# Optimization experiments

Measured on AMD Instinct MI355X. Metric: run time of the kernel, lower is better.

Reference implementation:

```python
import jax, jax.numpy as jnp
import numpy as np

H = 8  # number_heads

def setup_inputs() -> dict:
    key = jax.random.key(0)
    ks = jax.random.split(key, 10)
    B, Nx, Ny, Qd, Kd, Vd = 4, 2048, 2048, 512, 512, 512
    s = 0.02
    return {
        "X": jax.random.normal(ks[0], (B, Nx, Qd), jnp.float32),
        "Y": jax.random.normal(ks[1], (B, Ny, Kd), jnp.float32),
        "Wq": jax.random.normal(ks[2], (Vd, Qd), jnp.float32) * s,
        "bq": jax.random.normal(ks[3], (Vd,), jnp.float32) * s,
        "Wk": jax.random.normal(ks[4], (Vd, Kd), jnp.float32) * s,
        "bk": jax.random.normal(ks[5], (Vd,), jnp.float32) * s,
        "Wv": jax.random.normal(ks[6], (Vd, Kd), jnp.float32) * s,
        "bv": jax.random.normal(ks[7], (Vd,), jnp.float32) * s,
        "Wo": jax.random.normal(ks[8], (Vd, Vd), jnp.float32) * s,
        "bo": jax.random.normal(ks[9], (Vd,), jnp.float32) * s,
    }

def reference(X, Y, Wq, bq, Wk, bk, Wv, bv, Wo, bo):
    B, Nq, _ = X.shape
    Nk = Y.shape[1]
    Vd = Wq.shape[0]
    d = Vd // H  # head dim (dim_split)
    # QKV projections (torch Linear: x @ W^T + b)
    Q = (X @ Wq.T + bq).reshape(B, Nq, H, d)
    K = (Y @ Wk.T + bk).reshape(B, Nk, H, d)
    V = (Y @ Wv.T + bv).reshape(B, Nk, H, d)
    # attention: softmax(Q K^T / sqrt(d)) per head
    scores = jnp.einsum("bqhd,bkhd->bhqk", Q, K) / jnp.sqrt(jnp.float32(d))
    attn = jax.nn.softmax(scores, axis=-1)
    # residual on Q (pre-output-proj), per the original: O = Q_split + Attn @ V_split
    O = Q + jnp.einsum("bhqk,bkhd->bqhd", attn, V)
    O = O.reshape(B, Nq, Vd)  # concat heads back
    return O @ Wo.T + bo
```

## Files before the change

kernel.cpp:

```cpp
#include <hip/hip_runtime.h>
#include <hip/hip_bf16.h>

typedef unsigned short u16;
typedef __attribute__((ext_vector_type(4))) float f32x4;
typedef __attribute__((ext_vector_type(16))) float f32x16;
typedef __attribute__((ext_vector_type(8))) short bf16x8;
typedef __attribute__((ext_vector_type(4))) int i32x4;
typedef __attribute__((ext_vector_type(4))) unsigned short u16x4;

#define DEVI static __device__ __forceinline__

DEVI u16 f2bf(float f) {
  __hip_bfloat16 h = __float2bfloat16(f);
  return *reinterpret_cast<u16*>(&h);
}
DEVI float bf2f(u16 u) {
  unsigned int x = ((unsigned int)u) << 16;
  return __uint_as_float(x);
}
DEVI float exp2a(float x) {
  float r;
  asm("v_exp_f32 %0, %1" : "=v"(r) : "v"(x));
  return r;
}
DEVI int cvtpk(float lo, float hi) {
  int r;
  asm("v_cvt_pk_bf16_f32 %0, %1, %2" : "=v"(r) : "v"(lo), "v"(hi));
  return r;
}
DEVI f32x16 mfma32(bf16x8 a, bf16x8 b, f32x16 c) {
  return __builtin_amdgcn_mfma_f32_32x32x16_bf16(a, b, c, 0, 0, 0);
}
DEVI float xhalf_sum(float x) {
  float a = x, b;
  asm volatile("v_mov_b32 %0, %1" : "=v"(b) : "v"(x));
  asm volatile("v_permlane32_swap_b32 %0, %1" : "+v"(a), "+v"(b));
  return a + b;
}

DEVI void gload_lds16(const void* g, void* l) {
  __builtin_amdgcn_global_load_lds(
      (const __attribute__((address_space(1))) unsigned int*)g,
      (__attribute__((address_space(3))) unsigned int*)l, 16, 0, 0);
}

#define BAR() __builtin_amdgcn_s_barrier()
#define WAITV0() asm volatile("s_waitcnt vmcnt(0)" ::: "memory")
#define WAITV4() asm volatile("s_waitcnt vmcnt(4)" ::: "memory")
#define WAITV8() asm volatile("s_waitcnt vmcnt(8)" ::: "memory")

__global__ __launch_bounds__(256) void k_convall(
    const float* __restrict__ X, const float* __restrict__ Y,
    const float* __restrict__ Wq, const float* __restrict__ Wk,
    const float* __restrict__ Wv, const float* __restrict__ Wo,
    u16* __restrict__ Xb, u16* __restrict__ Yb, u16* __restrict__ Wb) {
  long i = ((long)blockIdx.x * 256 + threadIdx.x) * 8;
  const float* s;
  u16* d;
  long off;
  if (i < 4194304) {
    s = X; d = Xb; off = i;
  } else if (i < 8388608) {
    s = Y; d = Yb; off = i - 4194304;
  } else {
    long w = (i - 8388608) >> 18;
    off = (i - 8388608) & 262143;
    s = w == 0 ? Wq : w == 1 ? Wk : w == 2 ? Wv : Wo;
    d = Wb + w * 262144;
  }
  f32x4 a = *(const f32x4*)(s + off);
  f32x4 b = *(const f32x4*)(s + off + 4);
  bf16x8 v;
#pragma unroll
  for (int j = 0; j < 4; ++j) {
    v[j]     = (short)f2bf(a[j]);
    v[4 + j] = (short)f2bf(b[j]);
  }
  *(bf16x8*)(d + off) = v;
}

struct GemmAcc { f32x4 acc[4][4]; };

DEVI void gemm_body(const u16* __restrict__ A, const u16* __restrict__ Bw,
                    int m0, int n0, char* sm, GemmAcc& G) {
  const int tid = threadIdx.x;
  const int wid = tid >> 6, lane = tid & 63;
  const int g = lane >> 4, li = lane & 15;
  const int wr = wid >> 1, wc = wid & 1;

  int arow[4], acol[4];
#pragma unroll
  for (int i = 0; i < 4; ++i) {
    int P0 = ((i * 4 + wid) << 10) + lane * 16;
    int L0 = P0 ^ (((P0 >> 7) & 7) << 4);
    arow[i] = L0 >> 7;
    acol[i] = L0 & 127;
  }

#pragma unroll
  for (int mr = 0; mr < 4; ++mr)
#pragma unroll
    for (int nr = 0; nr < 4; ++nr) G.acc[mr][nr] = (f32x4){0.f, 0.f, 0.f, 0.f};

  auto stage = [&](int kt, int half) {
    char* As = sm + half * 32768;
    char* Bs = As + 16384;
    const int k0b = kt * 128;
#pragma unroll
    for (int i = 0; i < 4; ++i)
      gload_lds16((const char*)A + (size_t)(m0 + arow[i]) * 1024 + k0b + acol[i],
                  As + ((i * 4 + wid) << 10));
#pragma unroll
    for (int i = 0; i < 4; ++i)
      gload_lds16((const char*)Bw + (size_t)(n0 + arow[i]) * 1024 + k0b + acol[i],
                  Bs + ((i * 4 + wid) << 10));
  };

  stage(0, 0);
#pragma unroll 1
  for (int kt = 0; kt < 8; ++kt) {
    const int half = kt & 1;
    if (kt < 7) {
      stage(kt + 1, half ^ 1);
      WAITV8();
    } else {
      WAITV0();
    }
    BAR();
    const char* As = sm + half * 32768;
    const char* Bs = As + 16384;
#pragma unroll
    for (int ks = 0; ks < 2; ++ks) {
      bf16x8 af[4], bfr[4];
#pragma unroll
      for (int mr = 0; mr < 4; ++mr) {
        int row = wr * 64 + mr * 16 + li;
        int L = row * 128 + ks * 64 + g * 16;
        int P = L ^ ((row & 7) << 4);
        af[mr] = *(const bf16x8*)(As + P);
      }
#pragma unroll
      for (int nr = 0; nr < 4; ++nr) {
        int row = wc * 64 + nr * 16 + li;
        int L = row * 128 + ks * 64 + g * 16;
        int P = L ^ ((row & 7) << 4);
        bfr[nr] = *(const bf16x8*)(Bs + P);
      }
#pragma unroll
      for (int mr = 0; mr < 4; ++mr)
#pragma unroll
        for (int nr = 0; nr < 4; ++nr)
          G.acc[mr][nr] = __builtin_amdgcn_mfma_f32_16x16x32_bf16(
              af[mr], bfr[nr], G.acc[mr][nr], 0, 0, 0);
    }
    BAR();
  }
}

__global__ __launch_bounds__(256) void k_gemm_qkv(
    const u16* __restrict__ Xb, const u16* __restrict__ Yb,
    const u16* __restrict__ Wall, const float* __restrict__ bq,
    const float* __restrict__ bk, const float* __restrict__ bv,
    u16* __restrict__ Qb, u16* __restrict__ Kb, u16* __restrict__ Vtb) {
  __shared__ __align__(16) char sm[65536];
  const int z = blockIdx.z;
  int lin = blockIdx.x + 4 * blockIdx.y;
  int xcd = lin & 7, slot = lin >> 3;

  const u16 *Ag, *Bg;
  int m0, n0;
  if (z == 2) {
    Ag = Wall + 2 * 262144;
    Bg = Yb;
    m0 = (slot & 3) * 128;
    n0 = (xcd * 8 + (slot >> 2)) * 128;
  } else {
    Ag = z ? Yb : Xb;
    Bg = Wall + (size_t)z * 262144;
    m0 = (xcd * 8 + (slot >> 2)) * 128;
    n0 = (slot & 3) * 128;
  }

  GemmAcc G;
  gemm_body(Ag, Bg, m0, n0, sm, G);

  const int tid = threadIdx.x;
  const int wid = tid >> 6, lane = tid & 63;
  const int g = lane >> 4, li = lane & 15;
  const int wr = wid >> 1, wc = wid & 1;

  if (z <= 1) {
    u16* Cout = z ? Kb : Qb;
    const float* bias = z ? bk : bq;
#pragma unroll
    for (int nr = 0; nr < 4; ++nr) {
      int col = n0 + wc * 64 + nr * 16 + li;
      float bvv = bias[col];
#pragma unroll
      for (int mr = 0; mr < 4; ++mr) {
#pragma unroll
        for (int j = 0; j < 4; ++j) {
          int row = m0 + wr * 64 + mr * 16 + g * 4 + j;
          float v = G.acc[mr][nr][j] + bvv;
          int b = row >> 11, nn = row & 2047, h = col >> 6, dd = col & 63;
          Cout[(((size_t)(b * 8 + h) << 11) + nn) * 64 + dd] = f2bf(v);
        }
      }
    }
  } else {
#pragma unroll
    for (int mr = 0; mr < 4; ++mr) {
#pragma unroll
      for (int j = 0; j < 4; ++j) {
        int row = m0 + wr * 64 + mr * 16 + g * 4 + j;
        float bvv = bv[row];
        int hh = row >> 6, dd = row & 63;
#pragma unroll
        for (int nr = 0; nr < 4; ++nr) {
          int col = n0 + wc * 64 + nr * 16 + li;
          int b = col >> 11, nn = col & 2047;
          Vtb[(((size_t)(b * 8 + hh) * 64) + dd) * 2048 + nn] =
              f2bf(G.acc[mr][nr][j] + bvv);
        }
      }
    }
  }
}

__global__ __launch_bounds__(256) void k_gemm_out(const u16* __restrict__ A,
                                                  const u16* __restrict__ Bw,
                                                  const float* __restrict__ bias,
                                                  float* __restrict__ Cout) {
  __shared__ __align__(16) char sm[65536];
  int lin = blockIdx.x + 4 * blockIdx.y;
  int xcd = lin & 7, slot = lin >> 3;
  int by = xcd * 8 + (slot >> 2), bx = slot & 3;
  const int m0 = by * 128, n0 = bx * 128;

  GemmAcc G;
  gemm_body(A, Bw, m0, n0, sm, G);

  const int tid = threadIdx.x;
  const int wid = tid >> 6, lane = tid & 63;
  const int g = lane >> 4, li = lane & 15;
  const int wr = wid >> 1, wc = wid & 1;
#pragma unroll
  for (int nr = 0; nr < 4; ++nr) {
    int col = n0 + wc * 64 + nr * 16 + li;
    float bvv = bias[col];
#pragma unroll
    for (int mr = 0; mr < 4; ++mr) {
#pragma unroll
      for (int j = 0; j < 4; ++j) {
        int row = m0 + wr * 64 + mr * 16 + g * 4 + j;
        Cout[(size_t)row * 512 + col] = G.acc[mr][nr][j] + bvv;
      }
    }
  }
}

DEVI void attn_phase(const char* L, int kb, int vb, const int* v4, int sv0, int sv1,
                     const bf16x8* qfA, const bf16x8* qfB,
                     f32x16& oA0, f32x16& oA1, f32x16& oB0, f32x16& oB1,
                     float& lsumA, float& lsumB) {
  const f32x16 Z = {};
  f32x16 sA, sB;
  bf16x8 kf;
  kf = *(const bf16x8*)(L + kb + v4[0]);
  sA = mfma32(kf, qfA[0], Z);  sB = mfma32(kf, qfB[0], Z);
  kf = *(const bf16x8*)(L + kb + v4[1]);
  sA = mfma32(kf, qfA[1], sA); sB = mfma32(kf, qfB[1], sB);
  kf = *(const bf16x8*)(L + kb + v4[2]);
  sA = mfma32(kf, qfA[2], sA); sB = mfma32(kf, qfB[2], sB);
  kf = *(const bf16x8*)(L + kb + v4[3]);
  sA = mfma32(kf, qfA[3], sA); sB = mfma32(kf, qfB[3], sB);

  bf16x8 va0l = *(const bf16x8*)(L + vb + v4[sv0]);
  bf16x8 va0h = *(const bf16x8*)(L + vb + 4096 + v4[sv0]);
  bf16x8 va1l = *(const bf16x8*)(L + vb + v4[sv1]);
  bf16x8 va1h = *(const bf16x8*)(L + vb + 4096 + v4[sv1]);

#pragma unroll
  for (int i = 0; i < 16; ++i) sA[i] = exp2a(sA[i]);
#pragma unroll
  for (int i = 0; i < 16; ++i) sB[i] = exp2a(sB[i]);
  float tA[4], tB[4];
#pragma unroll
  for (int i = 0; i < 4; ++i) {
    tA[i] = (sA[4 * i] + sA[4 * i + 1]) + (sA[4 * i + 2] + sA[4 * i + 3]);
    tB[i] = (sB[4 * i] + sB[4 * i + 1]) + (sB[4 * i + 2] + sB[4 * i + 3]);
  }
  lsumA += (tA[0] + tA[1]) + (tA[2] + tA[3]);
  lsumB += (tB[0] + tB[1]) + (tB[2] + tB[3]);

  bf16x8 pbA[2], pbB[2];
#pragma unroll
  for (int kt = 0; kt < 2; ++kt) {
    const int base = kt * 8;
    int a0 = cvtpk(sA[base + 0], sA[base + 1]);
    int a1 = cvtpk(sA[base + 2], sA[base + 3]);
    int b0 = cvtpk(sA[base + 4], sA[base + 5]);
    int b1 = cvtpk(sA[base + 6], sA[base + 7]);
    asm volatile("v_permlane32_swap_b32 %0, %1" : "+v"(a0), "+v"(b0));
    asm volatile("v_permlane32_swap_b32 %0, %1" : "+v"(a1), "+v"(b1));
    i32x4 pi = {a0, a1, b0, b1};
    pbA[kt] = __builtin_bit_cast(bf16x8, pi);
    int c0 = cvtpk(sB[base + 0], sB[base + 1]);
    int c1 = cvtpk(sB[base + 2], sB[base + 3]);
    int d0 = cvtpk(sB[base + 4], sB[base + 5]);
    int d1 = cvtpk(sB[base + 6], sB[base + 7]);
    asm volatile("v_permlane32_swap_b32 %0, %1" : "+v"(c0), "+v"(d0));
    asm volatile("v_permlane32_swap_b32 %0, %1" : "+v"(c1), "+v"(d1));
    i32x4 qi = {c0, c1, d0, d1};
    pbB[kt] = __builtin_bit_cast(bf16x8, qi);
  }

  oA0 = mfma32(va0l, pbA[0], oA0);
  oB0 = mfma32(va0l, pbB[0], oB0);
  oA1 = mfma32(va0h, pbA[0], oA1);
  oB1 = mfma32(va0h, pbB[0], oB1);
  oA0 = mfma32(va1l, pbA[1], oA0);
  oB0 = mfma32(va1l, pbB[1], oB0);
  oA1 = mfma32(va1h, pbA[1], oA1);
  oB1 = mfma32(va1h, pbB[1], oB1);
}

__global__ __launch_bounds__(512, 2) void k_attn(const u16* __restrict__ Qb,
                                                 const u16* __restrict__ Kb,
                                                 const u16* __restrict__ Vt,
                                                 u16* __restrict__ Ob) {
  __shared__ __align__(16) char lds[67584];
  const int tid = threadIdx.x, wid = tid >> 6, lane = tid & 63;
  const int li = lane & 31, h = lane >> 5;
  const int grp = wid >> 2, w4 = wid & 3;

  const int lin = blockIdx.x;
  const int xcd = lin & 7, slot = lin >> 3;
  const int bh = xcd * 4 + (slot >> 3);
  const int qt = slot & 7;
  const int start = (slot * 3) & 15;

  const u16* Qh = Qb + ((size_t)bh << 11) * 64;
  const u16* Kh = Kb + ((size_t)bh << 11) * 64;
  const u16* Vh = Vt + (size_t)bh * 64 * 2048;

  int v4[4];
  {
    const int swz = (li & 7) << 4;
#pragma unroll
    for (int s = 0; s < 4; ++s) v4[s] = li * 128 + ((s * 32 + h * 16) ^ swz);
  }

  const int qA = qt * 256 + w4 * 64 + li;
  const int qB = qA + 32;
  const float C2 = 0.18033688f;
  bf16x8 qfA[4], qfB[4];
#pragma unroll
  for (int k4 = 0; k4 < 4; ++k4) {
    bf16x8 fA = *(const bf16x8*)(Qh + (size_t)qA * 64 + k4 * 16 + h * 8);
    bf16x8 fB = *(const bf16x8*)(Qh + (size_t)qB * 64 + k4 * 16 + h * 8);
    bf16x8 rA, rB;
#pragma unroll
    for (int e = 0; e < 4; ++e) {
      int pA = cvtpk(bf2f((u16)fA[2 * e]) * C2, bf2f((u16)fA[2 * e + 1]) * C2);
      rA[2 * e]     = (short)(pA & 0xffff);
      rA[2 * e + 1] = (short)((unsigned)pA >> 16);
      int pB = cvtpk(bf2f((u16)fB[2 * e]) * C2, bf2f((u16)fB[2 * e + 1]) * C2);
      rB[2 * e]     = (short)(pB & 0xffff);
      rB[2 * e + 1] = (short)((unsigned)pB >> 16);
    }
    qfA[k4] = rA;
    qfB[k4] = rB;
  }

  char* gb = lds + grp * 32768;
  const char* Lg = gb;
  int ksrc[2], vsrc[2];
#pragma unroll
  for (int j = 0; j < 2; ++j) {
    int P0 = w4 * 2048 + j * 1024 + lane * 16;
    int L0 = P0 ^ (((P0 >> 7) & 7) << 4);
    ksrc[j] = L0;
    vsrc[j] = (L0 >> 7) * 4096 + (L0 & 127);
  }

  auto T = [&](int n) { return grp * 16 + ((start + n) & 15); };
  auto stage = [&](int tt, int bb) {
#pragma unroll
    for (int j = 0; j < 2; ++j)
      gload_lds16((const char*)Kh + (size_t)tt * 8192 + ksrc[j],
                  gb + bb + w4 * 2048 + j * 1024);
#pragma unroll
    for (int j = 0; j < 2; ++j)
      gload_lds16((const char*)Vh + (size_t)tt * 128 + vsrc[j],
                  gb + bb + 8192 + w4 * 2048 + j * 1024);
  };

  f32x16 oA0 = {}, oA1 = {}, oB0 = {}, oB1 = {};
  float lsumA = 0.f, lsumB = 0.f;

  stage(T(0), 0);
  stage(T(1), 16384);
  WAITV4();
  BAR();

#pragma unroll 1
  for (int it = 0; it < 14; ++it) {
    const int cur = (it & 1) * 16384;
    attn_phase(Lg, cur, cur + 8192, v4, 0, 1, qfA, qfB, oA0, oA1, oB0, oB1,
               lsumA, lsumB);
    attn_phase(Lg, cur + 4096, cur + 8192, v4, 2, 3, qfA, qfB, oA0, oA1, oB0, oB1,
               lsumA, lsumB);
    BAR();
    stage(T(it + 2), cur);
    WAITV4();
    BAR();
  }
  attn_phase(Lg, 0, 8192, v4, 0, 1, qfA, qfB, oA0, oA1, oB0, oB1, lsumA, lsumB);
  attn_phase(Lg, 4096, 8192, v4, 2, 3, qfA, qfB, oA0, oA1, oB0, oB1, lsumA, lsumB);
  WAITV0();
  BAR();
  attn_phase(Lg, 16384, 24576, v4, 0, 1, qfA, qfB, oA0, oA1, oB0, oB1, lsumA, lsumB);
  attn_phase(Lg, 20480, 24576, v4, 2, 3, qfA, qfB, oA0, oA1, oB0, oB1, lsumA, lsumB);

  __syncthreads();
  if (grp == 1) {
#pragma unroll
    for (int j = 0; j < 16; ++j) {
      const f32x16& o = (j < 4) ? oA0 : (j < 8) ? oA1 : (j < 12) ? oB0 : oB1;
      const int s2 = (j & 3) * 4;
      f32x4 c = {o[s2 + 0], o[s2 + 1], o[s2 + 2], o[s2 + 3]};
      *(f32x4*)(lds + w4 * 16384 + j * 1024 + lane * 16) = c;
    }
    ((float*)(lds + 65536))[w4 * 128 + lane] = lsumA;
    ((float*)(lds + 65536))[w4 * 128 + 64 + lane] = lsumB;
  }
  __syncthreads();
  if (grp == 0) {
#pragma unroll
    for (int j = 0; j < 16; ++j) {
      f32x4 c = *(const f32x4*)(lds + w4 * 16384 + j * 1024 + lane * 16);
      f32x16& o = (j < 4) ? oA0 : (j < 8) ? oA1 : (j < 12) ? oB0 : oB1;
      const int s2 = (j & 3) * 4;
      o[s2 + 0] += c[0]; o[s2 + 1] += c[1]; o[s2 + 2] += c[2]; o[s2 + 3] += c[3];
    }
    lsumA += ((const float*)(lds + 65536))[w4 * 128 + lane];
    lsumB += ((const float*)(lds + 65536))[w4 * 128 + 64 + lane];
    const float invA = 1.0f / xhalf_sum(lsumA);
    const float invB = 1.0f / xhalf_sum(lsumB);

    const int b = bh >> 3, head = bh & 7;
#pragma unroll
    for (int half = 0; half < 2; ++half) {
      const int q = half ? qB : qA;
      const float inv = half ? invB : invA;
      u16* orow = Ob + ((size_t)(b * 2048 + q)) * 512 + head * 64;
      const u16* qrow = Qh + (size_t)q * 64;
#pragma unroll
      for (int dt = 0; dt < 2; ++dt) {
        const f32x16& o = half ? (dt ? oB1 : oB0) : (dt ? oA1 : oA0);
#pragma unroll
        for (int s2 = 0; s2 < 4; ++s2) {
          int d0 = dt * 32 + s2 * 8 + h * 4;
          u16x4 qv = *(const u16x4*)(qrow + d0);
          u16x4 w;
#pragma unroll
          for (int j = 0; j < 4; ++j)
            w[j] = f2bf(fmaf(o[s2 * 4 + j], inv, bf2f(qv[j])));
          *(u16x4*)(orow + d0) = w;
        }
      }
    }
  }
}

extern "C" void kernel_launch(void* const* d_in, const int* in_sizes, int n_in,
                              void* d_out, int out_size, void* d_ws, size_t ws_size,
                              hipStream_t stream) {
  const float* X  = (const float*)d_in[0];
  const float* Y  = (const float*)d_in[1];
  const float* Wq = (const float*)d_in[2];
  const float* bq = (const float*)d_in[3];
  const float* Wk = (const float*)d_in[4];
  const float* bk = (const float*)d_in[5];
  const float* Wv = (const float*)d_in[6];
  const float* bv = (const float*)d_in[7];
  const float* Wo = (const float*)d_in[8];
  const float* bo = (const float*)d_in[9];

  char* ws = (char*)d_ws;
  u16* Xb  = (u16*)(ws);
  u16* Yb  = (u16*)(ws + (size_t)(8  << 20));
  u16* Wb  = (u16*)(ws + (size_t)(16 << 20));
  u16* Qb  = (u16*)(ws + (size_t)(18 << 20));
  u16* Kb  = (u16*)(ws + (size_t)(26 << 20));
  u16* Vtb = (u16*)(ws + (size_t)(34 << 20));
  u16* Ob  = (u16*)(ws + (size_t)(42 << 20));

  k_convall<<<4608, 256, 0, stream>>>(X, Y, Wq, Wk, Wv, Wo, Xb, Yb, Wb);

  k_gemm_qkv<<<dim3(4, 64, 3), 256, 0, stream>>>(Xb, Yb, Wb, bq, bk, bv, Qb, Kb, Vtb);

  k_attn<<<256, 512, 0, stream>>>(Qb, Kb, Vtb, Ob);

  k_gemm_out<<<dim3(4, 64), 256, 0, stream>>>(Ob, Wb + 3 * 262144, bo, (float*)d_out);
}
```

Baseline: 84.73 us.

## Fuse fp32-to-bf16 conversion into GEMM loads, removing separate conversion kernel

Drops the standalone conversion pass that cast X, Y and all weights to bf16 in workspace. The GEMMs now load fp32 tiles into registers, pack them to bf16 and write them into swizzled LDS, with the next tile's global loads issued before the MFMA loop. This saves one launch and a full read-write pass over about 40 MB of activations. In exchange the GEMMs read twice the bytes, lose the async global-to-LDS path for fp32 operands, and wait on all loads plus LDS writes every k-step.

New measurement: 86.01 us. About the same (+1.5%).

```diff
diff --git a/kernel.cpp b/kernel.cpp
--- a/kernel.cpp
+++ b/kernel.cpp
@@ -47,54 +47,32 @@
 #define BAR() __builtin_amdgcn_s_barrier()
 #define WAITV0() asm volatile("s_waitcnt vmcnt(0)" ::: "memory")
 #define WAITV4() asm volatile("s_waitcnt vmcnt(4)" ::: "memory")
-#define WAITV8() asm volatile("s_waitcnt vmcnt(8)" ::: "memory")
-
-__global__ __launch_bounds__(256) void k_convall(
-    const float* __restrict__ X, const float* __restrict__ Y,
-    const float* __restrict__ Wq, const float* __restrict__ Wk,
-    const float* __restrict__ Wv, const float* __restrict__ Wo,
-    u16* __restrict__ Xb, u16* __restrict__ Yb, u16* __restrict__ Wb) {
-  long i = ((long)blockIdx.x * 256 + threadIdx.x) * 8;
-  const float* s;
-  u16* d;
-  long off;
-  if (i < 4194304) {
-    s = X; d = Xb; off = i;
-  } else if (i < 8388608) {
-    s = Y; d = Yb; off = i - 4194304;
-  } else {
-    long w = (i - 8388608) >> 18;
-    off = (i - 8388608) & 262143;
-    s = w == 0 ? Wq : w == 1 ? Wk : w == 2 ? Wv : Wo;
-    d = Wb + w * 262144;
-  }
-  f32x4 a = *(const f32x4*)(s + off);
-  f32x4 b = *(const f32x4*)(s + off + 4);
-  bf16x8 v;
-#pragma unroll
-  for (int j = 0; j < 4; ++j) {
-    v[j]     = (short)f2bf(a[j]);
-    v[4 + j] = (short)f2bf(b[j]);
-  }
-  *(bf16x8*)(d + off) = v;
-}
+#define WAITLGKM0() asm volatile("s_waitcnt lgkmcnt(0)" ::: "memory")
 
 struct GemmAcc { f32x4 acc[4][4]; };
 
-DEVI void gemm_body(const u16* __restrict__ A, const u16* __restrict__ Bw,
-                    int m0, int n0, char* sm, GemmAcc& G) {
+template <int AF, int BF>
+DEVI void gemm2(const char* A, const char* Bw, int m0, int n0, char* sm, GemmAcc& G) {
   const int tid = threadIdx.x;
   const int wid = tid >> 6, lane = tid & 63;
   const int g = lane >> 4, li = lane & 15;
   const int wr = wid >> 1, wc = wid & 1;
 
-  int arow[4], acol[4];
+  int brow[4], bcol[4];
 #pragma unroll
   for (int i = 0; i < 4; ++i) {
     int P0 = ((i * 4 + wid) << 10) + lane * 16;
     int L0 = P0 ^ (((P0 >> 7) & 7) << 4);
-    arow[i] = L0 >> 7;
-    acol[i] = L0 & 127;
+    brow[i] = L0 >> 7;
+    bcol[i] = L0 & 127;
+  }
+  int frow[4], fcol[4], fdst[4];
+#pragma unroll
+  for (int i = 0; i < 4; ++i) {
+    int c = tid + i * 256;
+    frow[i] = c >> 3;
+    fcol[i] = c & 7;
+    fdst[i] = (frow[i] * 128 + fcol[i] * 16) ^ ((frow[i] & 7) << 4);
   }
 
 #pragma unroll
@@ -102,31 +80,71 @@
 #pragma unroll
     for (int nr = 0; nr < 4; ++nr) G.acc[mr][nr] = (f32x4){0.f, 0.f, 0.f, 0.f};
 
-  auto stage = [&](int kt, int half) {
+  f32x4 ra[4][2], rb[4][2];
+
+  auto issue = [&](int kt, int half) {
     char* As = sm + half * 32768;
     char* Bs = As + 16384;
-    const int k0b = kt * 128;
-#pragma unroll
-    for (int i = 0; i < 4; ++i)
-      gload_lds16((const char*)A + (size_t)(m0 + arow[i]) * 1024 + k0b + acol[i],
-                  As + ((i * 4 + wid) << 10));
-#pragma unroll
-    for (int i = 0; i < 4; ++i)
-      gload_lds16((const char*)Bw + (size_t)(n0 + arow[i]) * 1024 + k0b + acol[i],
-                  Bs + ((i * 4 + wid) << 10));
+    const int k0 = kt * 64;
+    if (AF) {
+#pragma unroll
+      for (int i = 0; i < 4; ++i) {
+        const char* src = A + (size_t)(m0 + frow[i]) * 2048 + (size_t)(k0 + fcol[i] * 8) * 4;
+        ra[i][0] = *(const f32x4*)(src);
+        ra[i][1] = *(const f32x4*)(src + 16);
+      }
+    } else {
+#pragma unroll
+      for (int i = 0; i < 4; ++i)
+        gload_lds16(A + (size_t)(m0 + brow[i]) * 1024 + k0 * 2 + bcol[i],
+                    As + ((i * 4 + wid) << 10));
+    }
+    if (BF) {
+#pragma unroll
+      for (int i = 0; i < 4; ++i) {
+        const char* src = Bw + (size_t)(n0 + frow[i]) * 2048 + (size_t)(k0 + fcol[i] * 8) * 4;
+        rb[i][0] = *(const f32x4*)(src);
+        rb[i][1] = *(const f32x4*)(src + 16);
+      }
+    } else {
+#pragma unroll
+      for (int i = 0; i < 4; ++i)
+        gload_lds16(Bw + (size_t)(n0 + brow[i]) * 1024 + k0 * 2 + bcol[i],
+                    Bs + ((i * 4 + wid) << 10));
+    }
   };
 
-  stage(0, 0);
+  auto writeF = [&](int half) {
+    char* As = sm + half * 32768;
+    char* Bs = As + 16384;
+    if (AF) {
+#pragma unroll
+      for (int i = 0; i < 4; ++i) {
+        i32x4 w = {cvtpk(ra[i][0][0], ra[i][0][1]), cvtpk(ra[i][0][2], ra[i][0][3]),
+                   cvtpk(ra[i][1][0], ra[i][1][1]), cvtpk(ra[i][1][2], ra[i][1][3])};
+        *(i32x4*)(As + fdst[i]) = w;
+      }
+    }
+    if (BF) {
+#pragma unroll
+      for (int i = 0; i < 4; ++i) {
+        i32x4 w = {cvtpk(rb[i][0][0], rb[i][0][1]), cvtpk(rb[i][0][2], rb[i][0][3]),
+                   cvtpk(rb[i][1][0], rb[i][1][1]), cvtpk(rb[i][1][2], rb[i][1][3])};
+        *(i32x4*)(Bs + fdst[i]) = w;
+      }
+    }
+  };
+
+  issue(0, 0);
+  WAITV0();
+  writeF(0);
+  WAITLGKM0();
+  BAR();
+
 #pragma unroll 1
   for (int kt = 0; kt < 8; ++kt) {
     const int half = kt & 1;
-    if (kt < 7) {
-      stage(kt + 1, half ^ 1);
-      WAITV8();
-    } else {
-      WAITV0();
-    }
-    BAR();
+    if (kt < 7) issue(kt + 1, half ^ 1);
     const char* As = sm + half * 32768;
     const char* Bs = As + 16384;
 #pragma unroll
@@ -153,13 +171,19 @@
           G.acc[mr][nr] = __builtin_amdgcn_mfma_f32_16x16x32_bf16(
               af[mr], bfr[nr], G.acc[mr][nr], 0, 0, 0);
     }
+    if (kt < 7) {
+      WAITV0();
+      writeF(half ^ 1);
+      WAITLGKM0();
+    }
     BAR();
   }
 }
 
-__global__ __launch_bounds__(256) void k_gemm_qkv(
-    const u16* __restrict__ Xb, const u16* __restrict__ Yb,
-    const u16* __restrict__ Wall, const float* __restrict__ bq,
+__global__ __launch_bounds__(256, 1) void k_gemm_qkv(
+    const float* __restrict__ X, const float* __restrict__ Y,
+    const float* __restrict__ Wq, const float* __restrict__ Wk,
+    const float* __restrict__ Wv, const float* __restrict__ bq,
     const float* __restrict__ bk, const float* __restrict__ bv,
     u16* __restrict__ Qb, u16* __restrict__ Kb, u16* __restrict__ Vtb) {
   __shared__ __align__(16) char sm[65536];
@@ -167,22 +191,22 @@
   int lin = blockIdx.x + 4 * blockIdx.y;
   int xcd = lin & 7, slot = lin >> 3;
 
-  const u16 *Ag, *Bg;
+  const char *Ag, *Bg;
   int m0, n0;
   if (z == 2) {
-    Ag = Wall + 2 * 262144;
-    Bg = Yb;
+    Ag = (const char*)Wv;
+    Bg = (const char*)Y;
     m0 = (slot & 3) * 128;
     n0 = (xcd * 8 + (slot >> 2)) * 128;
   } else {
-    Ag = z ? Yb : Xb;
-    Bg = Wall + (size_t)z * 262144;
+    Ag = (const char*)(z ? Y : X);
+    Bg = (const char*)(z ? Wk : Wq);
     m0 = (xcd * 8 + (slot >> 2)) * 128;
     n0 = (slot & 3) * 128;
   }
 
   GemmAcc G;
-  gemm_body(Ag, Bg, m0, n0, sm, G);
+  gemm2<1, 1>(Ag, Bg, m0, n0, sm, G);
 
   const int tid = threadIdx.x;
   const int wid = tid >> 6, lane = tid & 63;
@@ -227,10 +251,10 @@
   }
 }
 
-__global__ __launch_bounds__(256) void k_gemm_out(const u16* __restrict__ A,
-                                                  const u16* __restrict__ Bw,
-                                                  const float* __restrict__ bias,
-                                                  float* __restrict__ Cout) {
+__global__ __launch_bounds__(256, 1) void k_gemm_out(const u16* __restrict__ A,
+                                                     const float* __restrict__ Wo,
+                                                     const float* __restrict__ bias,
+                                                     float* __restrict__ Cout) {
   __shared__ __align__(16) char sm[65536];
   int lin = blockIdx.x + 4 * blockIdx.y;
   int xcd = lin & 7, slot = lin >> 3;
@@ -238,7 +262,7 @@
   const int m0 = by * 128, n0 = bx * 128;
 
   GemmAcc G;
-  gemm_body(A, Bw, m0, n0, sm, G);
+  gemm2<0, 1>((const char*)A, (const char*)Wo, m0, n0, sm, G);
 
   const int tid = threadIdx.x;
   const int wid = tid >> 6, lane = tid & 63;
@@ -489,19 +513,15 @@
   const float* bo = (const float*)d_in[9];
 
   char* ws = (char*)d_ws;
-  u16* Xb  = (u16*)(ws);
-  u16* Yb  = (u16*)(ws + (size_t)(8  << 20));
-  u16* Wb  = (u16*)(ws + (size_t)(16 << 20));
-  u16* Qb  = (u16*)(ws + (size_t)(18 << 20));
-  u16* Kb  = (u16*)(ws + (size_t)(26 << 20));
-  u16* Vtb = (u16*)(ws + (size_t)(34 << 20));
-  u16* Ob  = (u16*)(ws + (size_t)(42 << 20));
-
-  k_convall<<<4608, 256, 0, stream>>>(X, Y, Wq, Wk, Wv, Wo, Xb, Yb, Wb);
-
-  k_gemm_qkv<<<dim3(4, 64, 3), 256, 0, stream>>>(Xb, Yb, Wb, bq, bk, bv, Qb, Kb, Vtb);
+  u16* Qb  = (u16*)(ws);
+  u16* Kb  = (u16*)(ws + (size_t)(8  << 20));
+  u16* Vtb = (u16*)(ws + (size_t)(16 << 20));
+  u16* Ob  = (u16*)(ws + (size_t)(24 << 20));
+
+  k_gemm_qkv<<<dim3(4, 64, 3), 256, 0, stream>>>(X, Y, Wq, Wk, Wv, bq, bk, bv,
+                                                 Qb, Kb, Vtb);
 
   k_attn<<<256, 512, 0, stream>>>(Qb, Kb, Vtb, Ob);
 
-  k_gemm_out<<<dim3(4, 64), 256, 0, stream>>>(Ob, Wb + 3 * 262144, bo, (float*)d_out);
-}
+  k_gemm_out<<<dim3(4, 64), 256, 0, stream>>>(Ob, Wo, bo, (float*)d_out);
+}
```
